# Optimization experiments

Measured on AMD Instinct MI355X. Metric: run time of the kernel, lower is better.

## Reference

```python
import jax, jax.numpy as jnp
import numpy as np

N_HEAD = 16


def setup_inputs() -> dict:
    key = jax.random.key(0)
    k1, k2, k3 = jax.random.split(key, 3)
    B, T, C = 4, 2048, 1024
    x = jax.random.normal(k1, (B, T, C), dtype=jnp.float32)
    W = jax.random.normal(k2, (3 * C, C), dtype=jnp.float32) * (1.0 / np.sqrt(C))
    b = jax.random.normal(k3, (3 * C,), dtype=jnp.float32) * 0.02
    return {"x": x, "W": W, "b": b, "input_pos": 0}


def reference(x, W, b, input_pos):
    # cache=False path; input_pos is unused (kept for signature fidelity).
    B, T, C = x.shape
    H = N_HEAD
    hs = C // H
    # Fused QKV projection: torch Linear is x @ W.T + b -> [B, T, 3C]
    qkv = (jnp.einsum('btc,oc->bto', x, W) + b).reshape(B, T, 3, H, hs)
    # q, k, v: [B, H, T, hs]
    q = jnp.transpose(qkv[:, :, 0], (0, 2, 1, 3))
    k = jnp.transpose(qkv[:, :, 1], (0, 2, 1, 3))
    v = jnp.transpose(qkv[:, :, 2], (0, 2, 1, 3))
    scale = hs ** (-0.5)
    # scores: [B, H, T, T]
    scores = jnp.einsum('bhqd,bhkd->bhqk', q, k) * scale
    causal = jnp.tril(jnp.ones((T, T), dtype=bool))
    scores = jnp.where(causal, scores, -jnp.inf)
    wei = jax.nn.softmax(scores, axis=-1)
    out = jnp.einsum('bhqk,bhkd->bhqd', wei, v)  # [B, H, T, hs]
    return jnp.transpose(out, (0, 2, 1, 3)).reshape(B, T, C)
```

## Files before the change

### kernel.cpp

```cpp
#include <hip/hip_runtime.h>
#include <stdint.h>

using s16x8 = __attribute__((ext_vector_type(8))) short;
using u16x8 = __attribute__((ext_vector_type(8))) unsigned short;
using f32x4 = __attribute__((ext_vector_type(4))) float;
using u32x2 = __attribute__((ext_vector_type(2))) uint32_t;

__device__ __forceinline__ unsigned short f2bf(float f) {
    union { float f; uint32_t u; } v; v.f = f;
    uint32_t u = (v.u + 0x7FFFu + ((v.u >> 16) & 1u)) >> 16;
    return (unsigned short)u;
}

__device__ __forceinline__ f32x4 zero4() { f32x4 z = {0.f, 0.f, 0.f, 0.f}; return z; }

__device__ __forceinline__ void async16(const void* g, void* l) {
    __builtin_amdgcn_global_load_lds(
        reinterpret_cast<const uint32_t __attribute__((address_space(1)))*>(
            reinterpret_cast<uintptr_t>(g)),
        reinterpret_cast<uint32_t __attribute__((address_space(3)))*>(
            (uint32_t)reinterpret_cast<uintptr_t>(l)),
        16, 0, 0);
}

__global__ void cvt_bf16(const float* __restrict__ in, unsigned short* __restrict__ out, int n) {
    int i = (blockIdx.x * 256 + threadIdx.x) * 8;
    if (i >= n) return;
    f32x4 a = *(const f32x4*)(in + i);
    f32x4 c = *(const f32x4*)(in + i + 4);
    u16x8 o;
    o[0] = f2bf(a[0]); o[1] = f2bf(a[1]); o[2] = f2bf(a[2]); o[3] = f2bf(a[3]);
    o[4] = f2bf(c[0]); o[5] = f2bf(c[1]); o[6] = f2bf(c[2]); o[7] = f2bf(c[3]);
    *(u16x8*)(out + i) = o;
}

#define SC 0.18033688011112042f

__global__ __launch_bounds__(256, 2)
void qkv_gemm(const unsigned short* __restrict__ A,
              const unsigned short* __restrict__ Bw,
              const float* __restrict__ bias,
              unsigned short* __restrict__ Qo,
              unsigned short* __restrict__ Ko,
              unsigned short* __restrict__ Vto) {
    constexpr int Kd = 1024, T = 2048, H = 16;
    __shared__ __align__(16) unsigned short smem[128 * 136];
    unsigned short* const As = smem;
    unsigned short* const Bs = smem + 128 * 64;
    const int tid = threadIdx.x;
    const int wave = tid >> 6, lane = tid & 63;
    const int q4 = lane >> 4, l15 = lane & 15;
    const int bm = blockIdx.y * 128, bn = blockIdx.x * 128;
    const int wm = (wave >> 1) * 64, wn = (wave & 1) * 64;

    f32x4 acc[4][4];
#pragma unroll
    for (int a = 0; a < 4; ++a)
#pragma unroll
        for (int c = 0; c < 4; ++c) acc[a][c] = zero4();

    for (int k0 = 0; k0 < Kd; k0 += 64) {
#pragma unroll
        for (int r = 0; r < 4; ++r) {
            int u = r * 256 + tid;
            int row = u >> 3, su = (u & 7) ^ (row & 7);
            async16(A + (size_t)(bm + row) * Kd + k0 + su * 8, (char*)As + u * 16);
        }
#pragma unroll
        for (int r = 0; r < 4; ++r) {
            int u = r * 256 + tid;
            int row = u >> 3, su = (u & 7) ^ (row & 7);
            async16(Bw + (size_t)(bn + row) * Kd + k0 + su * 8, (char*)Bs + u * 16);
        }
        __syncthreads();
#pragma unroll
        for (int kt = 0; kt < 2; ++kt) {
            s16x8 af[4];
#pragma unroll
            for (int mt = 0; mt < 4; ++mt) {
                int row = wm + mt * 16 + l15;
                int uu = (kt * 4 + q4) ^ (row & 7);
                af[mt] = *(const s16x8*)(As + row * 64 + uu * 8);
            }
#pragma unroll
            for (int nt = 0; nt < 4; ++nt) {
                int row = wn + nt * 16 + l15;
                int uu = (kt * 4 + q4) ^ (row & 7);
                s16x8 bfv = *(const s16x8*)(Bs + row * 64 + uu * 8);
#pragma unroll
                for (int mt = 0; mt < 4; ++mt)
                    acc[mt][nt] = __builtin_amdgcn_mfma_f32_16x16x32_bf16(af[mt], bfv, acc[mt][nt], 0, 0, 0);
            }
        }
        __syncthreads();
    }
    if (bn >= 2048) {
#pragma unroll
        for (int nt = 0; nt < 4; ++nt) {
            int n = bn + wn + nt * 16 + l15;
            float bv = bias[n];
            int dl = wn + nt * 16 + l15;
#pragma unroll
            for (int mt = 0; mt < 4; ++mt)
#pragma unroll
                for (int i = 0; i < 4; ++i) {
                    int ml = wm + mt * 16 + 4 * q4 + i;
                    smem[dl * 136 + ml] = f2bf(acc[mt][nt][i] + bv);
                }
        }
        __syncthreads();
        const int bb = bm >> 11, t0 = bm & (T - 1);
#pragma unroll
        for (int rr = 0; rr < 8; ++rr) {
            int r = wave * 32 + rr * 4 + q4;
            int d = (bn - 2048) + r;
            int h = d >> 6, dd = d & 63;
            u16x8 v = *(const u16x8*)(smem + r * 136 + l15 * 8);
            *(u16x8*)(Vto + (((size_t)(bb * H + h)) * 64 + dd) * T + t0 + l15 * 8) = v;
        }
    } else {
#pragma unroll
        for (int nt = 0; nt < 4; ++nt) {
            int n = bn + wn + nt * 16 + l15;
            float bv = bias[n];
            int which = n >> 10, h = (n >> 6) & (H - 1), d = n & 63;
            unsigned short* dst = (which == 0) ? Qo : Ko;
            float scl = (which == 0) ? SC : 1.0f;
#pragma unroll
            for (int mt = 0; mt < 4; ++mt)
#pragma unroll
                for (int i = 0; i < 4; ++i) {
                    int m = bm + wm + mt * 16 + 4 * q4 + i;
                    int bb = m >> 11, t = m & (T - 1);
                    dst[((((size_t)bb * H + h) * T) + t) * 64 + d] = f2bf((acc[mt][nt][i] + bv) * scl);
                }
        }
    }
}

__global__ __launch_bounds__(256, 3)
void flash_attn(const unsigned short* __restrict__ Qg,
                const unsigned short* __restrict__ Kg,
                const unsigned short* __restrict__ Vtg,
                float* __restrict__ Out) {
    constexpr int T = 2048;
    __shared__ __align__(16) unsigned short Qs[128 * 64];
    __shared__ __align__(16) unsigned short Ks[64 * 64];
    __shared__ __align__(16) unsigned short Vt[64 * 64];

    const int tid = threadIdx.x;
    const int wave = tid >> 6, lane = tid & 63;
    const int q4 = lane >> 4, l15 = lane & 15;
    const int bh = blockIdx.x;
    const int qt = (int)gridDim.y - 1 - (int)blockIdx.y;
    const int b = bh >> 4, h = bh & 15;
    const int q0 = qt * 128;
    const unsigned short* qb = Qg + (size_t)bh * T * 64;
    const unsigned short* kb = Kg + (size_t)bh * T * 64;
    const unsigned short* vtb = Vtg + (size_t)bh * 64 * T;

#pragma unroll
    for (int r = 0; r < 4; ++r) {
        int u = r * 256 + tid;
        int row = u >> 3, su = (u & 7) ^ (row & 7);
        async16(qb + (size_t)(q0 + row) * 64 + su * 8, (char*)Qs + u * 16);
    }
    __syncthreads();
    s16x8 aq[2][2];
#pragma unroll
    for (int s = 0; s < 2; ++s)
#pragma unroll
        for (int kt = 0; kt < 2; ++kt) {
            int arow = s * 64 + wave * 16 + l15;
            int au = (kt * 4 + q4) ^ (arow & 7);
            aq[s][kt] = *(const s16x8*)(Qs + arow * 64 + au * 8);
        }
    unsigned short* const Ps0 = Qs + (wave * 2 + 0) * 1024;
    unsigned short* const Ps1 = Qs + (wave * 2 + 1) * 1024;

    f32x4 oacc[2][4];
    float lsum[2] = {0.f, 0.f};
#pragma unroll
    for (int s = 0; s < 2; ++s)
#pragma unroll
        for (int ct = 0; ct < 4; ++ct) oacc[s][ct] = zero4();

    const int nkt = 2 * qt + 2;
    for (int j = 0; j < nkt; ++j) {
        const int c0 = j * 64;
#pragma unroll
        for (int r = 0; r < 2; ++r) {
            int u = r * 256 + tid;
            int row = u >> 3, su = (u & 7) ^ (row & 7);
            async16(kb + (size_t)(c0 + row) * 64 + su * 8, (char*)Ks + u * 16);
        }
#pragma unroll
        for (int r = 0; r < 2; ++r) {
            int u = r * 256 + tid;
            int row = u >> 3, su = (u & 7) ^ (row & 7);
            async16(vtb + (size_t)row * T + c0 + su * 8, (char*)Vt + u * 16);
        }
        __syncthreads();

        const bool alive0 = (j <= 2 * qt);

        f32x4 sv[2][4];
#pragma unroll
        for (int s = 0; s < 2; ++s)
#pragma unroll
            for (int t = 0; t < 4; ++t) sv[s][t] = zero4();
#pragma unroll
        for (int kt = 0; kt < 2; ++kt) {
#pragma unroll
            for (int t = 0; t < 4; ++t) {
                int krow = t * 16 + l15;
                int ku = (kt * 4 + q4) ^ (krow & 7);
                s16x8 ak = *(const s16x8*)(Ks + krow * 64 + ku * 8);
                sv[0][t] = __builtin_amdgcn_mfma_f32_16x16x32_bf16(ak, aq[0][kt], sv[0][t], 0, 0, 0);
                sv[1][t] = __builtin_amdgcn_mfma_f32_16x16x32_bf16(ak, aq[1][kt], sv[1][t], 0, 0, 0);
            }
        }

#pragma unroll
        for (int s = 0; s < 2; ++s) {
            if (s == 0 && !alive0) continue;
            const bool dg = (j == 2 * qt + s);
            unsigned short* const ps = (s == 0) ? Ps0 : Ps1;
            const int qrow = q0 + s * 64 + wave * 16 + l15;
#pragma unroll
            for (int t = 0; t < 4; ++t) {
                float p0 = exp2f(sv[s][t][0]);
                float p1 = exp2f(sv[s][t][1]);
                float p2 = exp2f(sv[s][t][2]);
                float p3 = exp2f(sv[s][t][3]);
                if (dg) {
                    int col = c0 + t * 16 + 4 * q4;
                    if (col + 0 > qrow) p0 = 0.f;
                    if (col + 1 > qrow) p1 = 0.f;
                    if (col + 2 > qrow) p2 = 0.f;
                    if (col + 3 > qrow) p3 = 0.f;
                }
                lsum[s] += (p0 + p1) + (p2 + p3);
                union { float f; uint32_t u; } a0, a1, a2, a3;
                a0.f = p0; a1.f = p1; a2.f = p2; a3.f = p3;
                u32x2 w;
                w[0] = ((a0.u + 0x8000u) >> 16) | ((a1.u + 0x8000u) & 0xffff0000u);
                w[1] = ((a2.u + 0x8000u) >> 16) | ((a3.u + 0x8000u) & 0xffff0000u);
                *(u32x2*)(ps + l15 * 64 + (((2 * t + (q4 >> 1)) ^ (l15 & 7)) << 3) +
                          ((q4 & 1) << 2)) = w;
            }
        }

#pragma unroll
        for (int kt = 0; kt < 2; ++kt) {
            int pu = ((kt * 4 + q4) ^ (l15 & 7)) * 8;
            s16x8 pa0, pa1;
            if (alive0) pa0 = *(const s16x8*)(Ps0 + l15 * 64 + pu);
            pa1 = *(const s16x8*)(Ps1 + l15 * 64 + pu);
#pragma unroll
            for (int ct = 0; ct < 4; ++ct) {
                int vrow = ct * 16 + l15;
                int vu = (kt * 4 + q4) ^ (vrow & 7);
                s16x8 vv = *(const s16x8*)(Vt + vrow * 64 + vu * 8);
                if (alive0)
                    oacc[0][ct] = __builtin_amdgcn_mfma_f32_16x16x32_bf16(pa0, vv, oacc[0][ct], 0, 0, 0);
                oacc[1][ct] = __builtin_amdgcn_mfma_f32_16x16x32_bf16(pa1, vv, oacc[1][ct], 0, 0, 0);
            }
        }
        __syncthreads();
    }
#pragma unroll
    for (int s = 0; s < 2; ++s) {
        float rs = lsum[s];
        rs += __shfl_xor(rs, 16, 64);
        rs += __shfl_xor(rs, 32, 64);
        float inv[4];
#pragma unroll
        for (int i = 0; i < 4; ++i)
            inv[i] = 1.0f / __shfl(rs, 4 * q4 + i, 64);
#pragma unroll
        for (int ct = 0; ct < 4; ++ct)
#pragma unroll
            for (int i = 0; i < 4; ++i) {
                int row = q0 + s * 64 + wave * 16 + 4 * q4 + i;
                Out[((size_t)b * T + row) * 1024 + h * 64 + ct * 16 + l15] =
                    oacc[s][ct][i] * inv[i];
            }
    }
}

extern "C" void kernel_launch(void* const* d_in, const int* in_sizes, int n_in,
                              void* d_out, int out_size, void* d_ws, size_t ws_size,
                              hipStream_t stream) {
    const float* x = (const float*)d_in[0];
    const float* W = (const float*)d_in[1];
    const float* bias = (const float*)d_in[2];
    float* out = (float*)d_out;

    unsigned short* xb = (unsigned short*)d_ws;
    unsigned short* wb = xb + 8388608;
    unsigned short* qb = wb + 3145728;
    unsigned short* kb = qb + 8388608;
    unsigned short* vtb = kb + 8388608;

    cvt_bf16<<<dim3(8388608 / 2048), dim3(256), 0, stream>>>(x, xb, 8388608);
    cvt_bf16<<<dim3(3145728 / 2048), dim3(256), 0, stream>>>(W, wb, 3145728);
    qkv_gemm<<<dim3(24, 64), dim3(256), 0, stream>>>(xb, wb, bias, qb, kb, vtb);
    flash_attn<<<dim3(64, 16), dim3(256), 0, stream>>>(qb, kb, vtb, out);
}
```

Baseline: 205.1 us.

## Double-buffer K/V tiles in flash attention and merge bf16 conversion launches

The attention loop now prefetches the next K and V^T tiles into a second LDS buffer with async global-to-LDS loads while the current tile is computed. This removes the per-iteration barrier that waited on loads before compute, so memory latency overlaps with the MFMA and softmax work. LDS use grows to 48KB per block, which may limit how many blocks fit per CU. Two smaller changes ride along: probabilities are packed to bf16 with a hardware packed-convert builtin when it exists (round-to-nearest-even instead of the old bit trick), and the two fp32-to-bf16 conversion kernels are merged into one launch.

Result: faster. 200.2 us (-2.4%).

```diff
diff --git a/kernel.cpp b/kernel.cpp
--- a/kernel.cpp
+++ b/kernel.cpp
@@ -10,6 +10,24 @@
     union { float f; uint32_t u; } v; v.f = f;
     uint32_t u = (v.u + 0x7FFFu + ((v.u >> 16) & 1u)) >> 16;
     return (unsigned short)u;
+}
+
+#if defined(__has_builtin)
+#if __has_builtin(__builtin_amdgcn_cvt_pk_bf16_f32)
+#define HAS_PK_BF16 1
+#endif
+#endif
+
+__device__ __forceinline__ uint32_t pk2bf(float x, float y) {
+#ifdef HAS_PK_BF16
+    typedef __bf16 bf16x2 __attribute__((ext_vector_type(2)));
+    union { bf16x2 v; uint32_t u; } c;
+    c.v = __builtin_amdgcn_cvt_pk_bf16_f32(x, y);
+    return c.u;
+#else
+    union { float f; uint32_t u; } a, b; a.f = x; b.f = y;
+    return ((a.u + 0x8000u) >> 16) | ((b.u + 0x8000u) & 0xffff0000u);
+#endif
 }
 
 __device__ __forceinline__ f32x4 zero4() { f32x4 z = {0.f, 0.f, 0.f, 0.f}; return z; }
@@ -23,15 +41,18 @@
         16, 0, 0);
 }
 
-__global__ void cvt_bf16(const float* __restrict__ in, unsigned short* __restrict__ out, int n) {
+__global__ void cvt_bf16_2(const float* __restrict__ xa, unsigned short* __restrict__ oa, int na,
+                           const float* __restrict__ xb, unsigned short* __restrict__ ob, int nb) {
     int i = (blockIdx.x * 256 + threadIdx.x) * 8;
-    if (i >= n) return;
-    f32x4 a = *(const f32x4*)(in + i);
-    f32x4 c = *(const f32x4*)(in + i + 4);
+    const float* in; unsigned short* out;
+    if (i < na) { in = xa + i; out = oa + i; }
+    else { int k = i - na; if (k >= nb) return; in = xb + k; out = ob + k; }
+    f32x4 a = *(const f32x4*)(in);
+    f32x4 c = *(const f32x4*)(in + 4);
     u16x8 o;
     o[0] = f2bf(a[0]); o[1] = f2bf(a[1]); o[2] = f2bf(a[2]); o[3] = f2bf(a[3]);
     o[4] = f2bf(c[0]); o[5] = f2bf(c[1]); o[6] = f2bf(c[2]); o[7] = f2bf(c[3]);
-    *(u16x8*)(out + i) = o;
+    *(u16x8*)(out) = o;
 }
 
 #define SC 0.18033688011112042f
@@ -145,8 +166,8 @@
                 float* __restrict__ Out) {
     constexpr int T = 2048;
     __shared__ __align__(16) unsigned short Qs[128 * 64];
-    __shared__ __align__(16) unsigned short Ks[64 * 64];
-    __shared__ __align__(16) unsigned short Vt[64 * 64];
+    __shared__ __align__(16) unsigned short Ks[2][64 * 64];
+    __shared__ __align__(16) unsigned short Vt[2][64 * 64];
 
     const int tid = threadIdx.x;
     const int wave = tid >> 6, lane = tid & 63;
@@ -165,6 +186,13 @@
         int row = u >> 3, su = (u & 7) ^ (row & 7);
         async16(qb + (size_t)(q0 + row) * 64 + su * 8, (char*)Qs + u * 16);
     }
+#pragma unroll
+    for (int r = 0; r < 2; ++r) {
+        int u = r * 256 + tid;
+        int row = u >> 3, su = (u & 7) ^ (row & 7);
+        async16(kb + (size_t)row * 64 + su * 8, (char*)Ks[0] + u * 16);
+        async16(vtb + (size_t)row * T + su * 8, (char*)Vt[0] + u * 16);
+    }
     __syncthreads();
     s16x8 aq[2][2];
 #pragma unroll
@@ -175,6 +203,7 @@
             int au = (kt * 4 + q4) ^ (arow & 7);
             aq[s][kt] = *(const s16x8*)(Qs + arow * 64 + au * 8);
         }
+    __syncthreads();
     unsigned short* const Ps0 = Qs + (wave * 2 + 0) * 1024;
     unsigned short* const Ps1 = Qs + (wave * 2 + 1) * 1024;
 
@@ -187,21 +216,21 @@
 
     const int nkt = 2 * qt + 2;
     for (int j = 0; j < nkt; ++j) {
+        if (j + 1 < nkt) {
+            const int cn = (j + 1) * 64;
+            unsigned short* kd = Ks[(j + 1) & 1];
+            unsigned short* vd = Vt[(j + 1) & 1];
+#pragma unroll
+            for (int r = 0; r < 2; ++r) {
+                int u = r * 256 + tid;
+                int row = u >> 3, su = (u & 7) ^ (row & 7);
+                async16(kb + (size_t)(cn + row) * 64 + su * 8, (char*)kd + u * 16);
+                async16(vtb + (size_t)row * T + cn + su * 8, (char*)vd + u * 16);
+            }
+        }
+        const unsigned short* kcur = Ks[j & 1];
+        const unsigned short* vcur = Vt[j & 1];
         const int c0 = j * 64;
-#pragma unroll
-        for (int r = 0; r < 2; ++r) {
-            int u = r * 256 + tid;
-            int row = u >> 3, su = (u & 7) ^ (row & 7);
-            async16(kb + (size_t)(c0 + row) * 64 + su * 8, (char*)Ks + u * 16);
-        }
-#pragma unroll
-        for (int r = 0; r < 2; ++r) {
-            int u = r * 256 + tid;
-            int row = u >> 3, su = (u & 7) ^ (row & 7);
-            async16(vtb + (size_t)row * T + c0 + su * 8, (char*)Vt + u * 16);
-        }
-        __syncthreads();
-
         const bool alive0 = (j <= 2 * qt);
 
         f32x4 sv[2][4];
@@ -215,7 +244,7 @@
             for (int t = 0; t < 4; ++t) {
                 int krow = t * 16 + l15;
                 int ku = (kt * 4 + q4) ^ (krow & 7);
-                s16x8 ak = *(const s16x8*)(Ks + krow * 64 + ku * 8);
+                s16x8 ak = *(const s16x8*)(kcur + krow * 64 + ku * 8);
                 sv[0][t] = __builtin_amdgcn_mfma_f32_16x16x32_bf16(ak, aq[0][kt], sv[0][t], 0, 0, 0);
                 sv[1][t] = __builtin_amdgcn_mfma_f32_16x16x32_bf16(ak, aq[1][kt], sv[1][t], 0, 0, 0);
             }
@@ -241,11 +270,9 @@
                     if (col + 3 > qrow) p3 = 0.f;
                 }
                 lsum[s] += (p0 + p1) + (p2 + p3);
-                union { float f; uint32_t u; } a0, a1, a2, a3;
-                a0.f = p0; a1.f = p1; a2.f = p2; a3.f = p3;
                 u32x2 w;
-                w[0] = ((a0.u + 0x8000u) >> 16) | ((a1.u + 0x8000u) & 0xffff0000u);
-                w[1] = ((a2.u + 0x8000u) >> 16) | ((a3.u + 0x8000u) & 0xffff0000u);
+                w[0] = pk2bf(p0, p1);
+                w[1] = pk2bf(p2, p3);
                 *(u32x2*)(ps + l15 * 64 + (((2 * t + (q4 >> 1)) ^ (l15 & 7)) << 3) +
                           ((q4 & 1) << 2)) = w;
             }
@@ -261,7 +288,7 @@
             for (int ct = 0; ct < 4; ++ct) {
                 int vrow = ct * 16 + l15;
                 int vu = (kt * 4 + q4) ^ (vrow & 7);
-                s16x8 vv = *(const s16x8*)(Vt + vrow * 64 + vu * 8);
+                s16x8 vv = *(const s16x8*)(vcur + vrow * 64 + vu * 8);
                 if (alive0)
                     oacc[0][ct] = __builtin_amdgcn_mfma_f32_16x16x32_bf16(pa0, vv, oacc[0][ct], 0, 0, 0);
                 oacc[1][ct] = __builtin_amdgcn_mfma_f32_16x16x32_bf16(pa1, vv, oacc[1][ct], 0, 0, 0);
@@ -303,8 +330,8 @@
     unsigned short* kb = qb + 8388608;
     unsigned short* vtb = kb + 8388608;
 
-    cvt_bf16<<<dim3(8388608 / 2048), dim3(256), 0, stream>>>(x, xb, 8388608);
-    cvt_bf16<<<dim3(3145728 / 2048), dim3(256), 0, stream>>>(W, wb, 3145728);
+    cvt_bf16_2<<<dim3((8388608 + 3145728) / 2048), dim3(256), 0, stream>>>(
+        x, xb, 8388608, W, wb, 3145728);
     qkv_gemm<<<dim3(24, 64), dim3(256), 0, stream>>>(xb, wb, bias, qb, kb, vtb);
     flash_attn<<<dim3(64, 16), dim3(256), 0, stream>>>(qb, kb, vtb, out);
 }
```
